# Kernel tuning notes

Hardware: AMD Instinct MI355X
Metric: run time of the kernel (lower is better)

Reference implementation:

```python
import jax, jax.numpy as jnp
import numpy as np

HIDDEN = 2048
HEADS = 16
HEAD_DIM = HIDDEN // HEADS  # 128
SCALE = 1.0 / float(np.sqrt(HEAD_DIM))
B, S = 2, 2048


def setup_inputs() -> dict:
    key = jax.random.key(0)
    ks = jax.random.split(key, 5)
    return {
        "x": jax.random.normal(ks[0], (B, S, HIDDEN), dtype=jnp.float32),
        "q_w": jax.random.normal(ks[1], (HIDDEN, HIDDEN), dtype=jnp.float32) * (HIDDEN ** -0.5),
        "k_w": jax.random.normal(ks[2], (HEAD_DIM, HIDDEN), dtype=jnp.float32) * (HIDDEN ** -0.5),
        "v_w": jax.random.normal(ks[3], (HEAD_DIM, HIDDEN), dtype=jnp.float32) * (HIDDEN ** -0.5),
        "o_w": jax.random.normal(ks[4], (HIDDEN, HIDDEN), dtype=jnp.float32) * (HIDDEN ** -0.5),
    }


def reference(x, q_w, k_w, v_w, o_w):
    b, s, _ = x.shape
    # torch F.linear: x @ W^T with W [out, in]
    q = (x @ q_w.T).reshape(b, s, HEADS, HEAD_DIM).transpose(0, 2, 1, 3)  # [B,H,S,D]
    k = x @ k_w.T  # [B,S,D] single shared KV head
    v = x @ v_w.T  # [B,S,D]
    # scores: [B,H,S,S] -- explicit O(S^2) materialization as in the source
    scores = jnp.einsum('bhqd,bkd->bhqk', q, k) * SCALE
    # softmax in float32 then cast back (matches dtype=torch.float32 then type_as)
    attn = jax.nn.softmax(scores.astype(jnp.float32), axis=-1).astype(q.dtype)
    out = jnp.einsum('bhqk,bkd->bhqd', attn, v)  # [B,H,S,D]
    out = out.transpose(0, 2, 1, 3).reshape(b, s, HIDDEN)
    return out @ o_w.T
```

## Files before the change

kernel.cpp:

```cpp
#include <hip/hip_runtime.h>
#include <stdint.h>

#define HID 2048
#define DHEAD 128
#define SEQL 2048
#define C2 0.1275187981510609f
#define MOFF 8.0f

typedef __attribute__((ext_vector_type(4))) float f32x4;
typedef __attribute__((ext_vector_type(8))) short s16x8;
typedef __attribute__((ext_vector_type(2))) unsigned int u32x2;

__device__ __forceinline__ unsigned short bf16_rne(float f) {
  union { float f; unsigned u; } v; v.f = f;
  return (unsigned short)((v.u + 0x7FFFu + ((v.u >> 16) & 1u)) >> 16);
}

__device__ __forceinline__ void gload_lds16(const void* g, void* l) {
  __builtin_amdgcn_global_load_lds(
      (__attribute__((address_space(1))) unsigned int*)(void*)g,
      (__attribute__((address_space(3))) unsigned int*)l, 16, 0, 0);
}

__device__ __forceinline__ void cvt8(const float* __restrict__ in,
                                     unsigned short* __restrict__ out, int k) {
  const f32x4* p = (const f32x4*)in;
  f32x4 a = p[2 * k], b = p[2 * k + 1];
  union { s16x8 v; unsigned short s[8]; } o;
  o.s[0] = bf16_rne(a[0]); o.s[1] = bf16_rne(a[1]);
  o.s[2] = bf16_rne(a[2]); o.s[3] = bf16_rne(a[3]);
  o.s[4] = bf16_rne(b[0]); o.s[5] = bf16_rne(b[1]);
  o.s[6] = bf16_rne(b[2]); o.s[7] = bf16_rne(b[3]);
  ((s16x8*)out)[k] = o.v;
}

__global__ __launch_bounds__(256) void cvt_bf16_k(const float* __restrict__ in,
                                                  unsigned short* __restrict__ out,
                                                  int n8) {
  int i = blockIdx.x * 256 + threadIdx.x;
  if (i >= n8) return;
  cvt8(in, out, i);
}

__global__ __launch_bounds__(256) void cvt4_k(
    const float* __restrict__ s0, unsigned short* __restrict__ d0, int n0,
    const float* __restrict__ s1, unsigned short* __restrict__ d1, int n1,
    const float* __restrict__ s2, unsigned short* __restrict__ d2, int n2,
    const float* __restrict__ s3, unsigned short* __restrict__ d3, int n3) {
  int i = blockIdx.x * 256 + threadIdx.x;
  if (i < n0) { cvt8(s0, d0, i); return; }
  i -= n0;
  if (i < n1) { cvt8(s1, d1, i); return; }
  i -= n1;
  if (i < n2) { cvt8(s2, d2, i); return; }
  i -= n2;
  if (i < n3) { cvt8(s3, d3, i); return; }
}

__global__ __launch_bounds__(256) void cvt5_k(
    const float* __restrict__ s0, unsigned short* __restrict__ d0, int n0,
    const float* __restrict__ s1, unsigned short* __restrict__ d1, int n1,
    const float* __restrict__ s2, unsigned short* __restrict__ d2, int n2,
    const float* __restrict__ s3, unsigned short* __restrict__ d3, int n3,
    const float* __restrict__ s4, unsigned short* __restrict__ d4, int n4) {
  int i = blockIdx.x * 256 + threadIdx.x;
  if (i < n0) { cvt8(s0, d0, i); return; }
  i -= n0;
  if (i < n1) { cvt8(s1, d1, i); return; }
  i -= n1;
  if (i < n2) { cvt8(s2, d2, i); return; }
  i -= n2;
  if (i < n3) { cvt8(s3, d3, i); return; }
  i -= n3;
  if (i < n4) { cvt8(s4, d4, i); return; }
}

__device__ __forceinline__ void stage_tile512(const unsigned short* __restrict__ src,
                                              int ld, char* smem, int t) {
#pragma unroll
  for (int i = 0; i < 2; ++i) {
    int c = i * 512 + t;
    int row = c >> 3;
    int slot = c & 7;
    gload_lds16(src + row * ld + ((slot ^ (row & 7)) << 3),
                smem + (i * 512 + (t >> 6) * 64) * 16);
  }
}

template <int MODE>
__global__ __launch_bounds__(512, 4) void gemm_bt(
    const unsigned short* __restrict__ A, const unsigned short* __restrict__ Bw,
    void* __restrict__ Cout, int M, int N, int K,
    unsigned short* __restrict__ Kb, unsigned short* __restrict__ Vt) {
  __shared__ char As[2][16384];
  __shared__ char Bs[2][16384];
  int t = threadIdx.x;
  int lane = t & 63, w = t >> 6;
  int wm = w >> 2, wn = w & 3;
  int l15 = lane & 15, l4 = lane >> 4;

  int gdx = gridDim.x;
  int nwg = gdx * gridDim.y;
  int bid = blockIdx.y * gdx + blockIdx.x;
  int q8 = nwg >> 3;
  int swz = (bid & 7) * q8 + (bid >> 3);
  int tm = (swz / gdx) * 128, tn = (swz % gdx) * 128;

  f32x4 acc[4][2] = {};

  stage_tile512(A + tm * K, K, As[0], t);
  stage_tile512(Bw + tn * K, K, Bs[0], t);
  stage_tile512(A + tm * K + 64, K, As[1], t);
  stage_tile512(Bw + tn * K + 64, K, Bs[1], t);

  int nk = K >> 6;
  for (int ki = 0; ki < nk; ++ki) {
    int cur = ki & 1;
    if (ki < nk - 1) asm volatile("s_waitcnt vmcnt(4)" ::: "memory");
    else             asm volatile("s_waitcnt vmcnt(0)" ::: "memory");
    __builtin_amdgcn_sched_barrier(0);
    __builtin_amdgcn_s_barrier();

    const char* as = As[cur];
    const char* bs = Bs[cur];
    s16x8 af[4][2], bfr[2][2];
#pragma unroll
    for (int m = 0; m < 4; ++m)
#pragma unroll
      for (int kk = 0; kk < 2; ++kk) {
        int row = wm * 64 + m * 16 + l15;
        af[m][kk] = *(const s16x8*)(as + row * 128 + (((kk * 4 + l4) ^ (row & 7)) << 4));
      }
#pragma unroll
    for (int n = 0; n < 2; ++n)
#pragma unroll
      for (int kk = 0; kk < 2; ++kk) {
        int row = wn * 32 + n * 16 + l15;
        bfr[n][kk] = *(const s16x8*)(bs + row * 128 + (((kk * 4 + l4) ^ (row & 7)) << 4));
      }
    asm volatile("s_waitcnt lgkmcnt(0)" ::: "memory");
    __builtin_amdgcn_sched_barrier(0);
    __builtin_amdgcn_s_barrier();
    if (ki + 2 < nk) {
      stage_tile512(A + tm * K + (ki + 2) * 64, K, As[cur], t);
      stage_tile512(Bw + tn * K + (ki + 2) * 64, K, Bs[cur], t);
    }
    __builtin_amdgcn_s_setprio(1);
#pragma unroll
    for (int m = 0; m < 4; ++m)
#pragma unroll
      for (int n = 0; n < 2; ++n)
#pragma unroll
        for (int kk = 0; kk < 2; ++kk)
          acc[m][n] = __builtin_amdgcn_mfma_f32_16x16x32_bf16(af[m][kk], bfr[n][kk],
                                                              acc[m][n], 0, 0, 0);
    __builtin_amdgcn_s_setprio(0);
  }

#pragma unroll
  for (int m = 0; m < 4; ++m)
#pragma unroll
    for (int n = 0; n < 2; ++n) {
      int col = tn + wn * 32 + n * 16 + l15;
#pragma unroll
      for (int j = 0; j < 4; ++j) {
        int row = tm + wm * 64 + m * 16 + l4 * 4 + j;
        float v = acc[m][n][j];
        if (MODE == 1) {
          ((float*)Cout)[row * N + col] = v;
        } else {
          if (col < 2048) {
            ((unsigned short*)Cout)[row * 2048 + col] = bf16_rne(v);
          } else if (col < 2176) {
            Kb[row * 128 + (col - 2048)] = bf16_rne(v);
          } else {
            int d = col - 2176, bb = row >> 11, s = row & 2047;
            Vt[((bb * 128 + d) << 11) + s] = bf16_rne(v);
          }
        }
      }
    }
}

__global__ __launch_bounds__(256, 2) void attn_k(
    const unsigned short* __restrict__ Q, const unsigned short* __restrict__ Kb,
    const unsigned short* __restrict__ Vt, unsigned short* __restrict__ AO) {
  __shared__ char Ks[2][16384];
  __shared__ char Vs[2][16384];
  __shared__ char Ps[4][4096];
  int t = threadIdx.x;
  int lane = t & 63, w = t >> 6;
  int l15 = lane & 15, l4 = lane >> 4;
  int qt = blockIdx.x, bh = blockIdx.y;
  int b = bh >> 4, h = bh & 15;
  int qg = b * SEQL + qt * 128 + w * 32;
  char* Psw = Ps[w];

  s16x8 qf[2][4];
#pragma unroll
  for (int m = 0; m < 2; ++m)
#pragma unroll
    for (int kc = 0; kc < 4; ++kc)
      qf[m][kc] = *(const s16x8*)(Q + (qg + m * 16 + l15) * HID + h * DHEAD + kc * 32 + l4 * 8);

  union { s16x8 v; unsigned short s[8]; } one_;
#pragma unroll
  for (int i = 0; i < 8; ++i) one_.s[i] = 0x3F80;
  const s16x8 ones = one_.v;

  f32x4 oacc[2][9] = {};

#pragma unroll
  for (int i = 0; i < 4; ++i) {
    int c = i * 256 + t, row = c >> 4, slot = c & 15;
    gload_lds16(Kb + (b * SEQL + row) * DHEAD + ((slot ^ (row & 7)) << 3),
                Ks[0] + (i * 256 + w * 64) * 16);
  }
#pragma unroll
  for (int i = 0; i < 4; ++i) {
    int c = i * 256 + t, row = c >> 3, slot = c & 7;
    gload_lds16(Vt + (b * DHEAD + row) * SEQL + ((slot ^ (row & 7)) << 3),
                Vs[0] + (i * 256 + w * 64) * 16);
  }
  asm volatile("s_waitcnt vmcnt(0)" ::: "memory");
  __builtin_amdgcn_s_barrier();

  for (int kv = 0; kv < SEQL; kv += 64) {
    int cur = (kv >> 6) & 1;
    if (kv + 64 < SEQL) {
#pragma unroll
      for (int i = 0; i < 4; ++i) {
        int c = i * 256 + t, row = c >> 4, slot = c & 15;
        gload_lds16(Kb + (b * SEQL + kv + 64 + row) * DHEAD + ((slot ^ (row & 7)) << 3),
                    Ks[cur ^ 1] + (i * 256 + w * 64) * 16);
      }
#pragma unroll
      for (int i = 0; i < 4; ++i) {
        int c = i * 256 + t, row = c >> 3, slot = c & 7;
        gload_lds16(Vt + (b * DHEAD + row) * SEQL + kv + 64 + ((slot ^ (row & 7)) << 3),
                    Vs[cur ^ 1] + (i * 256 + w * 64) * 16);
      }
    }

    const char* ks = Ks[cur];
    const char* vs = Vs[cur];

    f32x4 sacc[4][2] = {};
    __builtin_amdgcn_s_setprio(1);
#pragma unroll
    for (int n = 0; n < 4; ++n) {
      int krow = n * 16 + l15;
#pragma unroll
      for (int kc = 0; kc < 4; ++kc) {
        s16x8 kf = *(const s16x8*)(ks + krow * 256 + (((kc * 4 + l4) ^ (krow & 7)) << 4));
        sacc[n][0] = __builtin_amdgcn_mfma_f32_16x16x32_bf16(kf, qf[0][kc], sacc[n][0], 0, 0, 0);
        sacc[n][1] = __builtin_amdgcn_mfma_f32_16x16x32_bf16(kf, qf[1][kc], sacc[n][1], 0, 0, 0);
      }
    }
    __builtin_amdgcn_s_setprio(0);

#pragma unroll
    for (int m = 0; m < 2; ++m) {
      int q = m * 16 + l15;
      char* rowp = Psw + q * 128;
      int qx = q & 7;
#pragma unroll
      for (int n = 0; n < 4; ++n) {
        float p0 = __builtin_amdgcn_exp2f(__builtin_fmaf(sacc[n][m][0], C2, -MOFF));
        float p1 = __builtin_amdgcn_exp2f(__builtin_fmaf(sacc[n][m][1], C2, -MOFF));
        float p2 = __builtin_amdgcn_exp2f(__builtin_fmaf(sacc[n][m][2], C2, -MOFF));
        float p3 = __builtin_amdgcn_exp2f(__builtin_fmaf(sacc[n][m][3], C2, -MOFF));
        u32x2 pk;
        pk[0] = (unsigned)bf16_rne(p0) | ((unsigned)bf16_rne(p1) << 16);
        pk[1] = (unsigned)bf16_rne(p2) | ((unsigned)bf16_rne(p3) << 16);
        int off = (((2 * n + (l4 >> 1)) ^ qx) << 4) + ((l4 & 1) << 3);
        *(u32x2*)(rowp + off) = pk;
      }
    }

    asm volatile("s_waitcnt lgkmcnt(0)" ::: "memory");
    __builtin_amdgcn_sched_barrier(0);

#pragma unroll
    for (int kc2 = 0; kc2 < 2; ++kc2) {
      s16x8 pa[2];
#pragma unroll
      for (int m = 0; m < 2; ++m) {
        int row = m * 16 + l15;
        pa[m] = *(const s16x8*)(Psw + row * 128 + (((kc2 * 4 + l4) ^ (row & 7)) << 4));
      }
      __builtin_amdgcn_s_setprio(1);
#pragma unroll
      for (int n = 0; n < 8; ++n) {
        int vrow = n * 16 + l15;
        s16x8 vf = *(const s16x8*)(vs + vrow * 128 + (((kc2 * 4 + l4) ^ (vrow & 7)) << 4));
        oacc[0][n] = __builtin_amdgcn_mfma_f32_16x16x32_bf16(pa[0], vf, oacc[0][n], 0, 0, 0);
        oacc[1][n] = __builtin_amdgcn_mfma_f32_16x16x32_bf16(pa[1], vf, oacc[1][n], 0, 0, 0);
      }
      oacc[0][8] = __builtin_amdgcn_mfma_f32_16x16x32_bf16(pa[0], ones, oacc[0][8], 0, 0, 0);
      oacc[1][8] = __builtin_amdgcn_mfma_f32_16x16x32_bf16(pa[1], ones, oacc[1][8], 0, 0, 0);
      __builtin_amdgcn_s_setprio(0);
    }

    asm volatile("s_waitcnt vmcnt(0) lgkmcnt(0)" ::: "memory");
    __builtin_amdgcn_sched_barrier(0);
    __builtin_amdgcn_s_barrier();
  }

#pragma unroll
  for (int m = 0; m < 2; ++m) {
    float inv[4];
#pragma unroll
    for (int j = 0; j < 4; ++j) inv[j] = 1.f / oacc[m][8][j];
#pragma unroll
    for (int n = 0; n < 8; ++n) {
      int col = h * DHEAD + n * 16 + l15;
#pragma unroll
      for (int j = 0; j < 4; ++j) {
        int row = qg + m * 16 + l4 * 4 + j;
        AO[row * HID + col] = bf16_rne(oacc[m][n][j] * inv[j]);
      }
    }
  }
}

extern "C" void kernel_launch(void* const* d_in, const int* in_sizes, int n_in,
                              void* d_out, int out_size, void* d_ws, size_t ws_size,
                              hipStream_t stream) {
  const float* x  = (const float*)d_in[0];
  const float* qw = (const float*)d_in[1];
  const float* kw = (const float*)d_in[2];
  const float* vw = (const float*)d_in[3];
  const float* ow = (const float*)d_in[4];

  char* ws = (char*)d_ws;
  unsigned short* xb   = (unsigned short*)(ws);
  unsigned short* qwb  = (unsigned short*)(ws + 16777216);
  unsigned short* kvwb = (unsigned short*)(ws + 25165824);
  unsigned short* Qb   = (unsigned short*)(ws + 26214400);
  unsigned short* Kbuf = (unsigned short*)(ws + 42991616);
  unsigned short* Vtb  = (unsigned short*)(ws + 44040192);
  unsigned short* AOb  = xb;

  bool big = ws_size >= 54525953ull;
  unsigned short* owb = big ? (unsigned short*)(ws + 46137344) : qwb;

  if (big) {
    cvt5_k<<<8448, 256, 0, stream>>>(x, xb, 1048576, qw, qwb, 524288,
                                     kw, kvwb, 32768, vw, kvwb + 262144, 32768,
                                     ow, owb, 524288);
  } else {
    cvt4_k<<<6400, 256, 0, stream>>>(x, xb, 1048576, qw, qwb, 524288,
                                     kw, kvwb, 32768, vw, kvwb + 262144, 32768);
  }

  gemm_bt<0><<<dim3(18, 32), 512, 0, stream>>>(xb, qwb, Qb, 4096, 2304, 2048, Kbuf, Vtb);
  if (!big) {
    cvt_bf16_k<<<2048, 256, 0, stream>>>(ow, owb, 524288);
  }
  attn_k<<<dim3(16, 32), 256, 0, stream>>>(Qb, Kbuf, Vtb, AOb);
  gemm_bt<1><<<dim3(16, 32), 512, 0, stream>>>(AOb, owb, d_out, 4096, 2048, 2048,
                                               nullptr, nullptr);
}
```

Baseline: 195.0 us.

## Switch attention to 32x32x16 MFMA and keep P in registers via permlane swap

Rewrites the attention inner loop to use 32x32x16 bf16 MFMA tiles instead of 16x16x32. The S accumulator layout is rearranged with v_permlane32_swap so the exponentiated probabilities can feed the PV MFMA directly from registers, which removes the per-wave LDS scratch buffer, its stores and its reloads. bf16 conversion of P now truncates instead of rounding to nearest even. The larger accumulators raise register pressure and the output store pattern changes.

```diff
diff --git a/kernel.cpp b/kernel.cpp
--- a/kernel.cpp
+++ b/kernel.cpp
@@ -8,8 +8,8 @@
 #define MOFF 8.0f
 
 typedef __attribute__((ext_vector_type(4))) float f32x4;
+typedef __attribute__((ext_vector_type(16))) float f32x16;
 typedef __attribute__((ext_vector_type(8))) short s16x8;
-typedef __attribute__((ext_vector_type(2))) unsigned int u32x2;
 
 __device__ __forceinline__ unsigned short bf16_rne(float f) {
   union { float f; unsigned u; } v; v.f = f;
@@ -187,28 +187,25 @@
     const unsigned short* __restrict__ Vt, unsigned short* __restrict__ AO) {
   __shared__ char Ks[2][16384];
   __shared__ char Vs[2][16384];
-  __shared__ char Ps[4][4096];
   int t = threadIdx.x;
   int lane = t & 63, w = t >> 6;
-  int l15 = lane & 15, l4 = lane >> 4;
+  int l31 = lane & 31, lh = lane >> 5;
   int qt = blockIdx.x, bh = blockIdx.y;
   int b = bh >> 4, h = bh & 15;
   int qg = b * SEQL + qt * 128 + w * 32;
-  char* Psw = Ps[w];
-
-  s16x8 qf[2][4];
-#pragma unroll
-  for (int m = 0; m < 2; ++m)
-#pragma unroll
-    for (int kc = 0; kc < 4; ++kc)
-      qf[m][kc] = *(const s16x8*)(Q + (qg + m * 16 + l15) * HID + h * DHEAD + kc * 32 + l4 * 8);
+
+  s16x8 qf[8];
+#pragma unroll
+  for (int kc = 0; kc < 8; ++kc)
+    qf[kc] = *(const s16x8*)(Q + (qg + l31) * HID + h * DHEAD + kc * 16 + lh * 8);
 
   union { s16x8 v; unsigned short s[8]; } one_;
 #pragma unroll
   for (int i = 0; i < 8; ++i) one_.s[i] = 0x3F80;
-  const s16x8 ones = one_.v;
-
-  f32x4 oacc[2][9] = {};
+  const s16x8 onesb = one_.v;
+
+  f32x16 oacc[4] = {};
+  f32x16 dacc = {};
 
 #pragma unroll
   for (int i = 0; i < 4; ++i) {
@@ -245,83 +242,70 @@
     const char* ks = Ks[cur];
     const char* vs = Vs[cur];
 
-    f32x4 sacc[4][2] = {};
+    f32x16 s0 = {}, s1 = {};
     __builtin_amdgcn_s_setprio(1);
 #pragma unroll
-    for (int n = 0; n < 4; ++n) {
-      int krow = n * 16 + l15;
-#pragma unroll
-      for (int kc = 0; kc < 4; ++kc) {
-        s16x8 kf = *(const s16x8*)(ks + krow * 256 + (((kc * 4 + l4) ^ (krow & 7)) << 4));
-        sacc[n][0] = __builtin_amdgcn_mfma_f32_16x16x32_bf16(kf, qf[0][kc], sacc[n][0], 0, 0, 0);
-        sacc[n][1] = __builtin_amdgcn_mfma_f32_16x16x32_bf16(kf, qf[1][kc], sacc[n][1], 0, 0, 0);
-      }
+    for (int kc = 0; kc < 8; ++kc) {
+      int slot = kc * 2 + lh;
+      int r0 = l31, r1 = 32 + l31;
+      s16x8 kf0 = *(const s16x8*)(ks + r0 * 256 + ((slot ^ (r0 & 7)) << 4));
+      s16x8 kf1 = *(const s16x8*)(ks + r1 * 256 + ((slot ^ (r1 & 7)) << 4));
+      s0 = __builtin_amdgcn_mfma_f32_32x32x16_bf16(kf0, qf[kc], s0, 0, 0, 0);
+      s1 = __builtin_amdgcn_mfma_f32_32x32x16_bf16(kf1, qf[kc], s1, 0, 0, 0);
     }
     __builtin_amdgcn_s_setprio(0);
 
-#pragma unroll
-    for (int m = 0; m < 2; ++m) {
-      int q = m * 16 + l15;
-      char* rowp = Psw + q * 128;
-      int qx = q & 7;
-#pragma unroll
-      for (int n = 0; n < 4; ++n) {
-        float p0 = __builtin_amdgcn_exp2f(__builtin_fmaf(sacc[n][m][0], C2, -MOFF));
-        float p1 = __builtin_amdgcn_exp2f(__builtin_fmaf(sacc[n][m][1], C2, -MOFF));
-        float p2 = __builtin_amdgcn_exp2f(__builtin_fmaf(sacc[n][m][2], C2, -MOFF));
-        float p3 = __builtin_amdgcn_exp2f(__builtin_fmaf(sacc[n][m][3], C2, -MOFF));
-        u32x2 pk;
-        pk[0] = (unsigned)bf16_rne(p0) | ((unsigned)bf16_rne(p1) << 16);
-        pk[1] = (unsigned)bf16_rne(p2) | ((unsigned)bf16_rne(p3) << 16);
-        int off = (((2 * n + (l4 >> 1)) ^ qx) << 4) + ((l4 & 1) << 3);
-        *(u32x2*)(rowp + off) = pk;
-      }
-    }
-
-    asm volatile("s_waitcnt lgkmcnt(0)" ::: "memory");
-    __builtin_amdgcn_sched_barrier(0);
-
-#pragma unroll
-    for (int kc2 = 0; kc2 < 2; ++kc2) {
-      s16x8 pa[2];
-#pragma unroll
-      for (int m = 0; m < 2; ++m) {
-        int row = m * 16 + l15;
-        pa[m] = *(const s16x8*)(Psw + row * 128 + (((kc2 * 4 + l4) ^ (row & 7)) << 4));
-      }
-      __builtin_amdgcn_s_setprio(1);
-#pragma unroll
-      for (int n = 0; n < 8; ++n) {
-        int vrow = n * 16 + l15;
-        s16x8 vf = *(const s16x8*)(vs + vrow * 128 + (((kc2 * 4 + l4) ^ (vrow & 7)) << 4));
-        oacc[0][n] = __builtin_amdgcn_mfma_f32_16x16x32_bf16(pa[0], vf, oacc[0][n], 0, 0, 0);
-        oacc[1][n] = __builtin_amdgcn_mfma_f32_16x16x32_bf16(pa[1], vf, oacc[1][n], 0, 0, 0);
-      }
-      oacc[0][8] = __builtin_amdgcn_mfma_f32_16x16x32_bf16(pa[0], ones, oacc[0][8], 0, 0, 0);
-      oacc[1][8] = __builtin_amdgcn_mfma_f32_16x16x32_bf16(pa[1], ones, oacc[1][8], 0, 0, 0);
-      __builtin_amdgcn_s_setprio(0);
-    }
+    s16x8 paf[4];
+#pragma unroll
+    for (int g = 0; g < 2; ++g)
+#pragma unroll
+      for (int half = 0; half < 2; ++half) {
+        unsigned u[4];
+#pragma unroll
+        for (int i = 0; i < 4; ++i) {
+          float pe = __builtin_amdgcn_exp2f(__builtin_fmaf(
+              (g ? s1 : s0)[half * 8 + 2 * i], C2, -MOFF));
+          float po = __builtin_amdgcn_exp2f(__builtin_fmaf(
+              (g ? s1 : s0)[half * 8 + 2 * i + 1], C2, -MOFF));
+          u[i] = (__builtin_bit_cast(unsigned, po) & 0xFFFF0000u) |
+                 (__builtin_bit_cast(unsigned, pe) >> 16);
+        }
+        asm("v_permlane32_swap_b32 %0, %1" : "+v"(u[0]), "+v"(u[2]));
+        asm("v_permlane32_swap_b32 %0, %1" : "+v"(u[1]), "+v"(u[3]));
+        union { unsigned uu[4]; s16x8 v; } pk;
+        pk.uu[0] = u[0]; pk.uu[1] = u[1]; pk.uu[2] = u[2]; pk.uu[3] = u[3];
+        paf[g * 2 + half] = pk.v;
+      }
+
+    __builtin_amdgcn_s_setprio(1);
+#pragma unroll
+    for (int kstep = 0; kstep < 4; ++kstep) {
+#pragma unroll
+      for (int dg = 0; dg < 4; ++dg) {
+        int vrow = dg * 32 + l31;
+        int slot = kstep * 2 + lh;
+        s16x8 vf = *(const s16x8*)(vs + vrow * 128 + ((slot ^ (vrow & 7)) << 4));
+        oacc[dg] = __builtin_amdgcn_mfma_f32_32x32x16_bf16(paf[kstep], vf, oacc[dg], 0, 0, 0);
+      }
+      dacc = __builtin_amdgcn_mfma_f32_32x32x16_bf16(paf[kstep], onesb, dacc, 0, 0, 0);
+    }
+    __builtin_amdgcn_s_setprio(0);
 
     asm volatile("s_waitcnt vmcnt(0) lgkmcnt(0)" ::: "memory");
     __builtin_amdgcn_sched_barrier(0);
     __builtin_amdgcn_s_barrier();
   }
 
-#pragma unroll
-  for (int m = 0; m < 2; ++m) {
-    float inv[4];
-#pragma unroll
-    for (int j = 0; j < 4; ++j) inv[j] = 1.f / oacc[m][8][j];
-#pragma unroll
-    for (int n = 0; n < 8; ++n) {
-      int col = h * DHEAD + n * 16 + l15;
-#pragma unroll
-      for (int j = 0; j < 4; ++j) {
-        int row = qg + m * 16 + l4 * 4 + j;
-        AO[row * HID + col] = bf16_rne(oacc[m][n][j] * inv[j]);
-      }
-    }
-  }
+  float inv[16];
+#pragma unroll
+  for (int r = 0; r < 16; ++r) inv[r] = 1.f / dacc[r];
+#pragma unroll
+  for (int dg = 0; dg < 4; ++dg)
+#pragma unroll
+    for (int r = 0; r < 16; ++r) {
+      int qi = (r & 3) + 8 * (r >> 2) + 4 * lh;
+      AO[(qg + qi) * HID + h * DHEAD + dg * 32 + l31] = bf16_rne(oacc[dg][r] * inv[r]);
+    }
 }
 
 extern "C" void kernel_launch(void* const* d_in, const int* in_sizes, int n_in,
```

Result: no change. 194.8 us (-0.1%).
